# Optimization experiments

Hardware: AMD Instinct MI355X
Metric: run time of the kernel (lower is better)

The kernel has to match this reference:

```python
import jax, jax.numpy as jnp
import numpy as np

B, T, H, D = 256, 128, 256, 256
N_SUB = 2  # fixed-step RK4 substeps per observation interval (replaces adaptive odeint)


def setup_inputs() -> dict:
    key = jax.random.key(0)
    ks = jax.random.split(key, 16)
    # timestamps: strictly increasing, shared across batch (torch code uses b[0,:,0])
    times = jnp.cumsum(jax.random.uniform(ks[0], (T,), minval=0.05, maxval=0.15)) + 0.1
    vals = jax.random.uniform(ks[1], (B, T))
    b = jnp.stack([jnp.broadcast_to(times, (B, T)), vals], axis=-1)  # (B,T,2)
    u = jax.random.uniform(ks[2], (B, T))
    train_m = (u < 0.4).astype(jnp.float32)
    test_m = ((u >= 0.4) & (u < 0.7)).astype(jnp.float32)
    m = train_m + test_m  # disjoint -> in {0,1}
    h0 = jnp.zeros((B, H), jnp.float32)
    s = 0.05
    p = lambda k, shp: jax.random.normal(k, shp, jnp.float32) * s
    return {
        'b': b, 'm': m, 'train_m': train_m, 'test_m': test_m, 'h0': h0,
        # ODE func: Linear(H->D) then Linear(D->H) then tanh
        'W1': p(ks[3], (D, H)), 'b1': p(ks[4], (D,)),
        'W2': p(ks[5], (H, D)), 'b2': p(ks[6], (H,)),
        # GRUCell(input_size=1, hidden=H), torch layout (3H, in)
        'W_ih': p(ks[7], (3 * H, 1)), 'W_hh': p(ks[8], (3 * H, H)),
        'b_ih': p(ks[9], (3 * H,)), 'b_hh': p(ks[10], (3 * H,)),
        # output heads: Linear(H->D), Linear(D->1), tanh
        'Wo1': p(ks[11], (D, H)), 'bo1': p(ks[12], (D,)),
        'Wo2': p(ks[13], (1, D)), 'bo2': p(ks[14], (1,)),
    }


def _gru(x, h, W_ih, W_hh, b_ih, b_hh):
    gi = x @ W_ih.T + b_ih          # (B, 3H)
    gh = h @ W_hh.T + b_hh          # (B, 3H)
    i_r, i_z, i_n = jnp.split(gi, 3, axis=-1)
    h_r, h_z, h_n = jnp.split(gh, 3, axis=-1)
    r = jax.nn.sigmoid(i_r + h_r)
    z = jax.nn.sigmoid(i_z + h_z)
    n = jnp.tanh(i_n + r * h_n)
    return (1.0 - z) * n + z * h


def _ode_rnn(b, m, train_m, test_m, h0, W1, b1, W2, b2,
             W_ih, W_hh, b_ih, b_hh, Wo1, bo1, Wo2, bo2):
    f = lambda x: jnp.tanh((x @ W1.T + b1) @ W2.T + b2)  # autonomous ODE func

    def rk4(h, t0, t1):
        dt = (t1 - t0) / N_SUB
        def sub(h, _):
            k1 = f(h)
            k2 = f(h + 0.5 * dt * k1)
            k3 = f(h + 0.5 * dt * k2)
            k4 = f(h + dt * k3)
            return h + (dt / 6.0) * (k1 + 2.0 * k2 + 2.0 * k3 + k4), None
        h, _ = jax.lax.scan(sub, h, None, length=N_SUB)
        return h

    times = b[0, :, 0]                                      # (T,)
    t0s = jnp.concatenate([jnp.zeros((1,), times.dtype), times[:-1]])
    vals = b[:, :, 1]                                       # (B,T)

    def step(h, inp):
        t0, t1, bv, mv, trm, tem = inp
        hp = rk4(h, t0, t1)                                 # (B,H)
        out = jnp.tanh((hp @ Wo1.T + bo1) @ Wo2.T + bo2)[:, 0]  # (B,)
        htrain = _gru((bv * trm)[:, None], hp, W_ih, W_hh, b_ih, b_hh)
        htest = _gru((out * tem)[:, None], hp, W_ih, W_hh, b_ih, b_hh)
        h_new = trm[:, None] * htrain + tem[:, None] * htest + (1.0 - mv)[:, None] * hp
        return h_new, out

    xs = (t0s, times, vals.T, m.T, train_m.T, test_m.T)
    _, outs = jax.lax.scan(step, h0, xs)                    # outs: (T,B)
    return outs.T                                           # (B,T)


def reference(b, m, train_m, test_m, h0, W1, b1, W2, b2,
              W_ih, W_hh, b_ih, b_hh, Wo1, bo1, Wo2, bo2):
    return _ode_rnn(b, m, train_m, test_m, h0, W1, b1, W2, b2,
                    W_ih, W_hh, b_ih, b_hh, Wo1, bo1, Wo2, bo2)
```

## Files before the change

### kernel.cpp

```cpp
#include <hip/hip_runtime.h>

#define H 256
#define T_STEPS 128
#define B_BATCH 256
#define I_LDS 48
#define XGRP 36

__device__ __forceinline__ float sigmoidf_(float x) { return 1.0f / (1.0f + expf(-x)); }


__global__ void prep_weff(const float* __restrict__ W1, const float* __restrict__ W2,
                          const float* __restrict__ b1, const float* __restrict__ b2,
                          float* __restrict__ Weff, float* __restrict__ beff) {
    int i = blockIdx.x, j = threadIdx.x;
    const float* w2row = W2 + j * H;
    float acc = 0.f;
    for (int d = 0; d < H; ++d) acc += W1[d * H + i] * w2row[d];
    Weff[i * H + j] = acc;
    if (i == 0) {
        float bacc = b2[j];
        for (int d = 0; d < H; ++d) bacc += b1[d] * w2row[d];
        beff[j] = bacc;
    }
}

__global__ void prep_whht(const float* __restrict__ Whh, float* __restrict__ WhhT) {
    int idx = blockIdx.x * blockDim.x + threadIdx.x;
    int i = idx / 768;
    int r = idx - i * 768;
    WhhT[idx] = Whh[r * H + i];
}

__global__ void prep_wo(const float* __restrict__ Wo1, const float* __restrict__ Wo2,
                        const float* __restrict__ bo1, const float* __restrict__ bo2,
                        float* __restrict__ wo, float* __restrict__ bo) {
    int i = threadIdx.x;
    float acc = 0.f;
    for (int d = 0; d < H; ++d) acc += Wo1[d * H + i] * Wo2[d];
    wo[i] = acc;
    float p = bo1[i] * Wo2[i];
    __shared__ float red[4];
    for (int off = 32; off > 0; off >>= 1) p += __shfl_down(p, off);
    if ((i & 63) == 0) red[i >> 6] = p;
    __syncthreads();
    if (i == 0) bo[0] = red[0] + red[1] + red[2] + red[3] + bo2[0];
}


__global__ __attribute__((amdgpu_flat_work_group_size(1024, 1024),
                          amdgpu_waves_per_eu(4, 4)))
void ode_rnn_main(
    const float* __restrict__ b_in, const float* __restrict__ m_in,
    const float* __restrict__ trm_in, const float* __restrict__ tem_in,
    const float* __restrict__ h0,
    const float* __restrict__ Weff, const float* __restrict__ beff,
    const float* __restrict__ WhhT,
    const float* __restrict__ W_ih, const float* __restrict__ b_ih,
    const float* __restrict__ b_hh,
    const float* __restrict__ wo, const float* __restrict__ bo_p,
    float* __restrict__ out)
{
    const int tid = threadIdx.x;
    const int bb  = blockIdx.x;
    const int jp  = tid >> 3;
    const int e   = tid & 7;
    const int c   = e & 1;
    const int jc  = 2 * jp + c;

    __shared__ float whh_lds[I_LDS * 768];
    __shared__ __align__(16) float xsb[2][8 * XGRP];
    __shared__ __align__(16) float xsf[H];
    __shared__ float gh_lds[768];
    __shared__ float red[4];
    __shared__ float times_s[T_STEPS];
    __shared__ float bv_s[T_STEPS], trm_s[T_STEPS], tem_s[T_STEPS], m_s[T_STEPS];

    float2 wregv[32];
    #pragma unroll
    for (int il = 0; il < 32; ++il)
        wregv[il] = *(const float2*)&Weff[(32 * e + il) * H + 2 * jp];
    #pragma unroll
    for (int il = 0; il < 32; ++il)
        asm volatile("" : "+v"(wregv[il].x), "+v"(wregv[il].y));

    for (int k = tid; k < I_LDS * 768; k += 1024) whh_lds[k] = WhhT[k];
    if (tid < T_STEPS) {
        times_s[tid] = b_in[2 * tid];
        int bt = bb * T_STEPS + tid;
        bv_s[tid]  = b_in[2 * bt + 1];
        trm_s[tid] = trm_in[bt];
        tem_s[tid] = tem_in[bt];
        m_s[tid]   = m_in[bt];
    }

    float h = h0[bb * H + jc];
    const float be   = beff[jc];
    const float bihr = b_ih[jc], bihz = b_ih[H + jc], bihn = b_ih[2 * H + jc];
    const float bhhr = b_hh[jc], bhhz = b_hh[H + jc], bhhn = b_hh[2 * H + jc];
    const float wihr = W_ih[jc], wihz = W_ih[H + jc], wihn = W_ih[2 * H + jc];
    const float bo   = bo_p[0];
    const float wo_t = (tid >= 768) ? wo[tid - 768] : 0.f;

    const int pubpos = (jc >> 5) * XGRP + (jc & 31);

    if (e < 2) xsb[0][pubpos] = h;
    __syncthreads();

    #define EVAL(KOUT_) do {                                       \
        const float* xp_ = &xsb[cur][e * XGRP];                    \
        float a0_ = 0.f, a1_ = 0.f, b0_ = 0.f, b1_ = 0.f;          \
        _Pragma("unroll")                                          \
        for (int g_ = 0; g_ < 8; ++g_) {                           \
            float4 x_ = ((const float4*)xp_)[g_];                  \
            a0_ = fmaf(x_.x, wregv[4 * g_ + 0].x, a0_);            \
            b0_ = fmaf(x_.x, wregv[4 * g_ + 0].y, b0_);            \
            a1_ = fmaf(x_.y, wregv[4 * g_ + 1].x, a1_);            \
            b1_ = fmaf(x_.y, wregv[4 * g_ + 1].y, b1_);            \
            a0_ = fmaf(x_.z, wregv[4 * g_ + 2].x, a0_);            \
            b0_ = fmaf(x_.z, wregv[4 * g_ + 2].y, b0_);            \
            a1_ = fmaf(x_.w, wregv[4 * g_ + 3].x, a1_);            \
            b1_ = fmaf(x_.w, wregv[4 * g_ + 3].y, b1_);            \
        }                                                          \
        float s0_ = a0_ + a1_, s1_ = b0_ + b1_;                    \
        _Pragma("unroll")                                          \
        for (int o_ = 1; o_ < 8; o_ <<= 1) {                       \
            s0_ += __shfl_xor(s0_, o_);                            \
            s1_ += __shfl_xor(s1_, o_);                            \
        }                                                          \
        KOUT_ = tanhf(be + (c == 0 ? s0_ : s1_));                  \
    } while (0)

    #define PUBLISH(V_) do {                                       \
        if (e < 2) xsb[cur ^ 1][pubpos] = (V_);                    \
        __syncthreads();                                           \
        cur ^= 1;                                                  \
    } while (0)

    float tprev = 0.f;
    #pragma unroll 1
    for (int t = 0; t < T_STEPS; ++t) {
        float t1 = times_s[t];
        float dt = (t1 - tprev) * 0.5f;
        tprev = t1;

        int cur = 0;
        float k1, k2, k3, k4;
        #pragma unroll 1
        for (int s = 0; s < 2; ++s) {
            EVAL(k1); PUBLISH(fmaf(0.5f * dt, k1, h));
            EVAL(k2); PUBLISH(fmaf(0.5f * dt, k2, h));
            EVAL(k3); PUBLISH(fmaf(dt, k3, h));
            EVAL(k4);
            h = fmaf(dt * (1.f / 6.f), k1 + 2.f * (k2 + k3) + k4, h);
            if (s == 0) PUBLISH(h);
        }

        if (e < 2) xsf[jc] = h;
        __syncthreads();

        if (tid < 768) {
            float g0 = 0.f, g1 = 0.f, g2 = 0.f, g3 = 0.f;
            const float* wl = whh_lds + tid;
            #pragma unroll 4
            for (int i = 0; i < I_LDS; i += 4) {
                float4 xv = *(const float4*)(xsf + i);
                g0 = fmaf(xv.x, wl[(i + 0) * 768], g0);
                g1 = fmaf(xv.y, wl[(i + 1) * 768], g1);
                g2 = fmaf(xv.z, wl[(i + 2) * 768], g2);
                g3 = fmaf(xv.w, wl[(i + 3) * 768], g3);
            }
            const float* wr = WhhT + I_LDS * 768 + tid;
            #pragma unroll 8
            for (int i = 0; i < H - I_LDS; i += 4) {
                float4 xv = *(const float4*)(xsf + I_LDS + i);
                g0 = fmaf(xv.x, wr[(i + 0) * 768], g0);
                g1 = fmaf(xv.y, wr[(i + 1) * 768], g1);
                g2 = fmaf(xv.z, wr[(i + 2) * 768], g2);
                g3 = fmaf(xv.w, wr[(i + 3) * 768], g3);
            }
            gh_lds[tid] = (g0 + g1) + (g2 + g3);
        } else {
            float p = xsf[tid - 768] * wo_t;
            #pragma unroll
            for (int off = 32; off > 0; off >>= 1) p += __shfl_down(p, off);
            if ((tid & 63) == 0) red[(tid - 768) >> 6] = p;
        }
        __syncthreads();

        {
            float outv = tanhf(red[0] + red[1] + red[2] + red[3] + bo);
            float bv = bv_s[t], trm = trm_s[t], tem = tem_s[t], mv = m_s[t];
            float ghr = gh_lds[jc] + bhhr;
            float ghz = gh_lds[256 + jc] + bhhz;
            float ghn = gh_lds[512 + jc] + bhhn;
            float x1v = bv * trm, x2v = outv * tem;

            float r1 = sigmoidf_(fmaf(x1v, wihr, bihr) + ghr);
            float z1 = sigmoidf_(fmaf(x1v, wihz, bihz) + ghz);
            float n1 = tanhf(fmaf(x1v, wihn, bihn) + r1 * ghn);
            float h1 = (1.f - z1) * n1 + z1 * h;

            float r2 = sigmoidf_(fmaf(x2v, wihr, bihr) + ghr);
            float z2 = sigmoidf_(fmaf(x2v, wihz, bihz) + ghz);
            float n2 = tanhf(fmaf(x2v, wihn, bihn) + r2 * ghn);
            float h2 = (1.f - z2) * n2 + z2 * h;

            if (tid == 0) out[bb * T_STEPS + t] = outv;
            h = trm * h1 + tem * h2 + (1.f - mv) * h;
        }

        if (e < 2) xsb[0][pubpos] = h;
        __syncthreads();
    }
    #undef EVAL
    #undef PUBLISH
}


extern "C" void kernel_launch(void* const* d_in, const int* in_sizes, int n_in,
                              void* d_out, int out_size, void* d_ws, size_t ws_size,
                              hipStream_t stream) {
    const float* b_in = (const float*)d_in[0];
    const float* m_in = (const float*)d_in[1];
    const float* trm  = (const float*)d_in[2];
    const float* tem  = (const float*)d_in[3];
    const float* h0   = (const float*)d_in[4];
    const float* W1   = (const float*)d_in[5];
    const float* b1   = (const float*)d_in[6];
    const float* W2   = (const float*)d_in[7];
    const float* b2   = (const float*)d_in[8];
    const float* W_ih = (const float*)d_in[9];
    const float* W_hh = (const float*)d_in[10];
    const float* b_ih = (const float*)d_in[11];
    const float* b_hh = (const float*)d_in[12];
    const float* Wo1  = (const float*)d_in[13];
    const float* bo1  = (const float*)d_in[14];
    const float* Wo2  = (const float*)d_in[15];
    const float* bo2  = (const float*)d_in[16];

    float* ws   = (float*)d_ws;
    float* Weff = ws;
    float* beff = Weff + 65536;
    float* WhhT = beff + 256;
    float* wo   = WhhT + 196608;
    float* bo   = wo + 256;

    prep_weff<<<256, 256, 0, stream>>>(W1, W2, b1, b2, Weff, beff);
    prep_whht<<<192, 1024, 0, stream>>>(W_hh, WhhT);
    prep_wo<<<1, 256, 0, stream>>>(Wo1, Wo2, bo1, bo2, wo, bo);

    ode_rnn_main<<<B_BATCH, 1024, 0, stream>>>(b_in, m_in, trm, tem, h0,
                                               Weff, beff, WhhT,
                                               W_ih, b_ih, b_hh, wo, bo,
                                               (float*)d_out);
}
```

Measured before the change: 2.169 ms.

## Use fast exp2/rcp activations, trim shuffle reduction, vectorize GRU W_hh matvec

Replaces libm tanhf/expf with clamped hardware exp2 and reciprocal-with-Newton-step versions. Cuts the EVAL shuffle reduction from six to four cross-lane ops by exchanging partial sums. Rewrites the GRU W_hh matvec so each thread loads float4 weight rows across four interleaved input slices and combines them with xor shuffles, aiming for wider, more coalesced global/LDS loads. Accuracy of the fast transcendentals is slightly lower, and the new access pattern relies on the transposed layout.

```diff
diff --git a/kernel.cpp b/kernel.cpp
--- a/kernel.cpp
+++ b/kernel.cpp
@@ -6,7 +6,32 @@
 #define I_LDS 48
 #define XGRP 36
 
-__device__ __forceinline__ float sigmoidf_(float x) { return 1.0f / (1.0f + expf(-x)); }
+#define LOG2E 1.4426950408889634f
+
+__device__ __forceinline__ float fexp2_(float x) {
+#if __has_builtin(__builtin_amdgcn_exp2f)
+    return __builtin_amdgcn_exp2f(x);
+#else
+    return exp2f(x);
+#endif
+}
+__device__ __forceinline__ float frcp_(float x) {
+#if __has_builtin(__builtin_amdgcn_rcpf)
+    float r = __builtin_amdgcn_rcpf(x);
+    return r * (2.0f - x * r);
+#else
+    return 1.0f / x;
+#endif
+}
+__device__ __forceinline__ float tanhf_(float x) {
+    float xc = fminf(fmaxf(x, -16.f), 16.f);
+    float t  = fexp2_(xc * (2.f * LOG2E));
+    return (t - 1.f) * frcp_(t + 1.f);
+}
+__device__ __forceinline__ float sigmoidf_(float x) {
+    float xc = fminf(fmaxf(x, -30.f), 30.f);
+    return frcp_(1.f + fexp2_(-xc * LOG2E));
+}
 
 
 __global__ void prep_weff(const float* __restrict__ W1, const float* __restrict__ W2,
@@ -101,6 +126,9 @@
     const float bo   = bo_p[0];
     const float wo_t = (tid >= 768) ? wo[tid - 768] : 0.f;
 
+    const int rq = tid >> 2;
+    const int is = tid & 3;
+
     const int pubpos = (jc >> 5) * XGRP + (jc & 31);
 
     if (e < 2) xsb[0][pubpos] = h;
@@ -122,12 +150,12 @@
             b1_ = fmaf(x_.w, wregv[4 * g_ + 3].y, b1_);            \
         }                                                          \
         float s0_ = a0_ + a1_, s1_ = b0_ + b1_;                    \
-        _Pragma("unroll")                                          \
-        for (int o_ = 1; o_ < 8; o_ <<= 1) {                       \
-            s0_ += __shfl_xor(s0_, o_);                            \
-            s1_ += __shfl_xor(s1_, o_);                            \
-        }                                                          \
-        KOUT_ = tanhf(be + (c == 0 ? s0_ : s1_));                  \
+        float v_ = (c == 0) ? s0_ : s1_;                           \
+        float u_ = (c == 0) ? s1_ : s0_;                           \
+        v_ += __shfl_xor(u_, 1);                                   \
+        v_ += __shfl_xor(v_, 2);                                   \
+        v_ += __shfl_xor(v_, 4);                                   \
+        KOUT_ = tanhf_(be + v_);                                   \
     } while (0)
 
     #define PUBLISH(V_) do {                                       \
@@ -159,26 +187,40 @@
         __syncthreads();
 
         if (tid < 768) {
-            float g0 = 0.f, g1 = 0.f, g2 = 0.f, g3 = 0.f;
-            const float* wl = whh_lds + tid;
-            #pragma unroll 4
-            for (int i = 0; i < I_LDS; i += 4) {
-                float4 xv = *(const float4*)(xsf + i);
-                g0 = fmaf(xv.x, wl[(i + 0) * 768], g0);
-                g1 = fmaf(xv.y, wl[(i + 1) * 768], g1);
-                g2 = fmaf(xv.z, wl[(i + 2) * 768], g2);
-                g3 = fmaf(xv.w, wl[(i + 3) * 768], g3);
+            float4 acc = {0.f, 0.f, 0.f, 0.f};
+            {
+                const float* wbase = WhhT + is * 768 + 4 * rq;
+                #pragma unroll 8
+                for (int ii = 12; ii < 64; ++ii) {
+                    float  x = xsf[4 * ii + is];
+                    float4 w = *(const float4*)(wbase + ii * 4 * 768);
+                    acc.x = fmaf(x, w.x, acc.x);
+                    acc.y = fmaf(x, w.y, acc.y);
+                    acc.z = fmaf(x, w.z, acc.z);
+                    acc.w = fmaf(x, w.w, acc.w);
+                }
             }
-            const float* wr = WhhT + I_LDS * 768 + tid;
-            #pragma unroll 8
-            for (int i = 0; i < H - I_LDS; i += 4) {
-                float4 xv = *(const float4*)(xsf + I_LDS + i);
-                g0 = fmaf(xv.x, wr[(i + 0) * 768], g0);
-                g1 = fmaf(xv.y, wr[(i + 1) * 768], g1);
-                g2 = fmaf(xv.z, wr[(i + 2) * 768], g2);
-                g3 = fmaf(xv.w, wr[(i + 3) * 768], g3);
+            {
+                const float* lbase = whh_lds + is * 768 + 4 * rq;
+                #pragma unroll 4
+                for (int ii = 0; ii < 12; ++ii) {
+                    float  x = xsf[4 * ii + is];
+                    float4 w = *(const float4*)(lbase + ii * 4 * 768);
+                    acc.x = fmaf(x, w.x, acc.x);
+                    acc.y = fmaf(x, w.y, acc.y);
+                    acc.z = fmaf(x, w.z, acc.z);
+                    acc.w = fmaf(x, w.w, acc.w);
+                }
             }
-            gh_lds[tid] = (g0 + g1) + (g2 + g3);
+            #pragma unroll
+            for (int o_ = 1; o_ < 4; o_ <<= 1) {
+                acc.x += __shfl_xor(acc.x, o_);
+                acc.y += __shfl_xor(acc.y, o_);
+                acc.z += __shfl_xor(acc.z, o_);
+                acc.w += __shfl_xor(acc.w, o_);
+            }
+            float ov = (is == 0) ? acc.x : (is == 1) ? acc.y : (is == 2) ? acc.z : acc.w;
+            gh_lds[4 * rq + is] = ov;
         } else {
             float p = xsf[tid - 768] * wo_t;
             #pragma unroll
@@ -188,7 +230,7 @@
         __syncthreads();
 
         {
-            float outv = tanhf(red[0] + red[1] + red[2] + red[3] + bo);
+            float outv = tanhf_(red[0] + red[1] + red[2] + red[3] + bo);
             float bv = bv_s[t], trm = trm_s[t], tem = tem_s[t], mv = m_s[t];
             float ghr = gh_lds[jc] + bhhr;
             float ghz = gh_lds[256 + jc] + bhhz;
@@ -197,12 +239,12 @@
 
             float r1 = sigmoidf_(fmaf(x1v, wihr, bihr) + ghr);
             float z1 = sigmoidf_(fmaf(x1v, wihz, bihz) + ghz);
-            float n1 = tanhf(fmaf(x1v, wihn, bihn) + r1 * ghn);
+            float n1 = tanhf_(fmaf(x1v, wihn, bihn) + r1 * ghn);
             float h1 = (1.f - z1) * n1 + z1 * h;
 
             float r2 = sigmoidf_(fmaf(x2v, wihr, bihr) + ghr);
             float z2 = sigmoidf_(fmaf(x2v, wihz, bihz) + ghz);
-            float n2 = tanhf(fmaf(x2v, wihn, bihn) + r2 * ghn);
+            float n2 = tanhf_(fmaf(x2v, wihn, bihn) + r2 * ghn);
             float h2 = (1.f - z2) * n2 + z2 * h;
 
             if (tid == 0) out[bb * T_STEPS + t] = outv;
```

New measurement: 3.106 ms. 1.43x slower.
